# Kernel tuning notes

Measured on AMD Instinct MI355X. Metric: run time of the kernel, lower is better.

## Reference

```python
import jax, jax.numpy as jnp
import numpy as np

EMBED = 1024
HEADS = 16
HEAD_DIM = EMBED // HEADS
N, L = 2, 2048


def setup_inputs() -> dict:
    key = jax.random.key(0)
    ks = jax.random.split(key, 9)
    s = 0.02
    return {
        "values": jax.random.normal(ks[0], (N, L, EMBED), jnp.float32),
        "key": jax.random.normal(ks[1], (N, L, EMBED), jnp.float32),
        "query": jax.random.normal(ks[2], (N, L, EMBED), jnp.float32),
        "mask": jnp.ones((N, 1, 1, L), jnp.int32),
        "Wv": jax.random.normal(ks[3], (HEAD_DIM, HEAD_DIM), jnp.float32) * s,
        "Wk": jax.random.normal(ks[4], (HEAD_DIM, HEAD_DIM), jnp.float32) * s,
        "Wq": jax.random.normal(ks[5], (HEAD_DIM, HEAD_DIM), jnp.float32) * s,
        "bq": jax.random.normal(ks[6], (HEAD_DIM,), jnp.float32) * s,
        "Wo": jax.random.normal(ks[7], (EMBED, EMBED), jnp.float32) * s,
        "bo": jax.random.normal(ks[8], (EMBED,), jnp.float32) * s,
    }


def reference(values, key, query, mask, Wv, Wk, Wq, bq, Wo, bo):
    n, q_len, E = query.shape
    D = Wv.shape[0]
    H = E // D
    # split heads: (N, len, H, D)
    v = values.reshape(n, -1, H, D)
    k = key.reshape(n, -1, H, D)
    q = query.reshape(n, q_len, H, D)
    # per-head linear projections (torch Linear: x @ W.T [+ b])
    v = jnp.einsum("nlhd,ed->nlhe", v, Wv)
    k = jnp.einsum("nlhd,ed->nlhe", k, Wk)
    q = jnp.einsum("nlhd,ed->nlhe", q, Wq) + bq
    # scores: (N, H, q_len, k_len)
    energy = jnp.einsum("nqhd,nkhd->nhqk", q, k)
    energy = jnp.where(mask == 0, jnp.float32(-1e20), energy)
    # NOTE: original scales by sqrt(embed_size), not sqrt(head_dim)
    attn = jax.nn.softmax(energy / jnp.sqrt(jnp.float32(E)), axis=-1)
    out = jnp.einsum("nhqk,nkhd->nqhd", attn, v).reshape(n, q_len, E)
    return out @ Wo.T + bo
```

## Files before the change

kernel.cpp:

```cpp
#include <hip/hip_runtime.h>
#include <hip/hip_bf16.h>
#include <string.h>

#define NB   2
#define SEQ  2048
#define EMB  1024
#define NH   16
#define HD   64
#define SCALE 0.03125f
#define MADD  -3.125e18f

typedef __attribute__((ext_vector_type(8))) short short8;
typedef __attribute__((ext_vector_type(4))) float f32x4;

#define MFMA(a, b, c) __builtin_amdgcn_mfma_f32_16x16x32_bf16(a, b, c, 0, 0, 0)

__device__ __forceinline__ unsigned short f2bf(float x) {
    union { float f; unsigned u; } v; v.f = x;
    unsigned r = v.u + 0x7fffu + ((v.u >> 16) & 1u);
    return (unsigned short)(r >> 16);
}
__device__ __forceinline__ unsigned packbf2(float a, float b) {
    __hip_bfloat162 h = __float22bfloat162_rn(make_float2(a, b));
    unsigned u; memcpy(&u, &h, 4);
    return u;
}

__global__ __launch_bounds__(256) void cvt_wo_kernel(
    const float* __restrict__ Wo, unsigned short* __restrict__ Wob)
{
    int idx = blockIdx.x * 256 + threadIdx.x;
    float4 w = ((const float4*)Wo)[idx];
    uint2 p; p.x = packbf2(w.x, w.y); p.y = packbf2(w.z, w.w);
    ((uint2*)Wob)[idx] = p;
}

__global__ __launch_bounds__(256) void qkv_kernel(
    const float* __restrict__ Qin, const float* __restrict__ Kin,
    const float* __restrict__ Vin,
    const float* __restrict__ Wq, const float* __restrict__ Wk,
    const float* __restrict__ Wv, const float* __restrict__ bq,
    unsigned short* __restrict__ Qp, unsigned short* __restrict__ Kp,
    unsigned short* __restrict__ Vtp)
{
    const int lt = blockIdx.x;
    const int h  = blockIdx.y;
    const int tz = blockIdx.z;
    const int t  = tz >> 1;
    const int n  = tz & 1;

    const float* X; const float* W;
    if (t == 0)      { X = Qin; W = Wq; }
    else if (t == 1) { X = Kin; W = Wk; }
    else             { X = Vin; W = Wv; }

    __shared__ __align__(16) unsigned short sX[64][72];
    __shared__ __align__(16) unsigned short sW[64][72];
    __shared__ __align__(16) unsigned short sT[64][72];

    const int tid  = threadIdx.x;
    const int wave = tid >> 6, lane = tid & 63;
    const int ln   = lane & 15, quad = lane >> 4;

    #pragma unroll
    for (int i = 0; i < 4; ++i) {
        int flat = tid + i * 256;
        int r = flat >> 4, c4 = flat & 15;
        float4 xv = *(const float4*)(X + ((size_t)(n * SEQ + lt * 64 + r)) * EMB + h * HD + c4 * 4);
        uint2 xp; xp.x = packbf2(xv.x, xv.y); xp.y = packbf2(xv.z, xv.w);
        *(uint2*)&sX[r][c4 * 4] = xp;
        float4 wv = *(const float4*)(W + r * HD + c4 * 4);
        uint2 wp; wp.x = packbf2(wv.x, wv.y); wp.y = packbf2(wv.z, wv.w);
        *(uint2*)&sW[r][c4 * 4] = wp;
    }
    __syncthreads();

    short8 af0 = *(const short8*)&sX[wave * 16 + ln][quad * 8];
    short8 af1 = *(const short8*)&sX[wave * 16 + ln][32 + quad * 8];

    f32x4 acc[4];
    #pragma unroll
    for (int nt = 0; nt < 4; ++nt) {
        short8 bf0 = *(const short8*)&sW[nt * 16 + ln][quad * 8];
        short8 bf1 = *(const short8*)&sW[nt * 16 + ln][32 + quad * 8];
        f32x4 a = {0.f, 0.f, 0.f, 0.f};
        a = MFMA(af0, bf0, a);
        a = MFMA(af1, bf1, a);
        acc[nt] = a;
    }

    if (t == 0) {
        #pragma unroll
        for (int nt = 0; nt < 4; ++nt) {
            float bb = bq[nt * 16 + ln];
            #pragma unroll
            for (int a = 0; a < 4; ++a) acc[nt][a] = (acc[nt][a] + bb) * SCALE;
        }
    }

    if (t < 2) {
        unsigned short* Out = (t == 0) ? Qp : Kp;
        #pragma unroll
        for (int a = 0; a < 4; ++a) {
            size_t row = (size_t)((n * NH + h) * SEQ + lt * 64 + wave * 16 + quad * 4 + a);
            #pragma unroll
            for (int nt = 0; nt < 4; ++nt)
                Out[row * HD + nt * 16 + ln] = f2bf(acc[nt][a]);
        }
    } else {
        #pragma unroll
        for (int nt = 0; nt < 4; ++nt)
            #pragma unroll
            for (int a = 0; a < 4; ++a)
                sT[nt * 16 + ln][wave * 16 + quad * 4 + a] = f2bf(acc[nt][a]);
        __syncthreads();
        #pragma unroll
        for (int i = 0; i < 2; ++i) {
            int flat = tid + i * 256;
            int r = flat >> 3, c8 = flat & 7;
            *(float4*)(Vtp + ((size_t)((n * NH + h) * HD + r)) * SEQ + lt * 64 + c8 * 8) =
                *(const float4*)&sT[r][c8 * 8];
        }
    }
}

__global__ __launch_bounds__(128, 2) void flash_kernel(
    const unsigned short* __restrict__ Qp, const unsigned short* __restrict__ Kp,
    const unsigned short* __restrict__ Vtp, const int* __restrict__ mask,
    unsigned short* __restrict__ A )
{
    const int nh = blockIdx.x;
    const int qt = blockIdx.y;
    const int n  = nh >> 4, h = nh & 15;

    const int tid  = threadIdx.x;
    const int wave = tid >> 6, lane = tid & 63;
    const int ln   = lane & 15, quad = lane >> 4;

    __shared__ __align__(16) unsigned short sK [64][72];
    __shared__ __align__(16) unsigned short sVt[64][72];
    __shared__ __align__(16) unsigned short sP [64][72];
    __shared__ float sMadd[SEQ];

    for (int i = tid; i < SEQ; i += 128)
        sMadd[i] = mask[n * SEQ + i] ? 0.f : MADD;

    const unsigned short* Qb = Qp + ((size_t)nh * SEQ + qt * 64 + wave * 32) * HD;
    short8 qf0[2], qf1[2];
    #pragma unroll
    for (int set = 0; set < 2; ++set) {
        qf0[set] = *(const short8*)(Qb + (set * 16 + ln) * HD + quad * 8);
        qf1[set] = *(const short8*)(Qb + (set * 16 + ln) * HD + 32 + quad * 8);
    }

    const unsigned short* Kb = Kp  + (size_t)nh * SEQ * HD;
    const unsigned short* Vb = Vtp + (size_t)nh * HD * SEQ;

    f32x4 o[2][4];
    #pragma unroll
    for (int s2 = 0; s2 < 2; ++s2)
        #pragma unroll
        for (int dt = 0; dt < 4; ++dt) o[s2][dt] = (f32x4){0.f, 0.f, 0.f, 0.f};
    float lsum[2] = {0.f, 0.f};

    for (int kt = 0; kt < SEQ / 64; ++kt) {
        __syncthreads();
        #pragma unroll
        for (int i = 0; i < 4; ++i) {
            int flat = tid + i * 128; int r = flat >> 3, c8 = flat & 7;
            *(float4*)&sK [r][c8 * 8] = *(const float4*)(Kb + ((size_t)(kt * 64 + r)) * HD + c8 * 8);
            *(float4*)&sVt[r][c8 * 8] = *(const float4*)(Vb + (size_t)r * SEQ + kt * 64 + c8 * 8);
        }
        __syncthreads();

        f32x4 s[2][4];
        #pragma unroll
        for (int nt = 0; nt < 4; ++nt) {
            short8 kf0 = *(const short8*)&sK[nt * 16 + ln][quad * 8];
            short8 kf1 = *(const short8*)&sK[nt * 16 + ln][32 + quad * 8];
            f32x4 z0 = {0.f, 0.f, 0.f, 0.f};
            f32x4 z1 = {0.f, 0.f, 0.f, 0.f};
            z0 = MFMA(kf0, qf0[0], z0);
            z0 = MFMA(kf1, qf1[0], z0);
            z1 = MFMA(kf0, qf0[1], z1);
            z1 = MFMA(kf1, qf1[1], z1);
            s[0][nt] = z0; s[1][nt] = z1;
        }

        #pragma unroll
        for (int set = 0; set < 2; ++set) {
            #pragma unroll
            for (int nt = 0; nt < 4; ++nt) {
                float4 md = *(const float4*)&sMadd[kt * 64 + nt * 16 + quad * 4];
                float p0 = __expf(fminf(s[set][nt][0] + md.x, 60.f));
                float p1 = __expf(fminf(s[set][nt][1] + md.y, 60.f));
                float p2 = __expf(fminf(s[set][nt][2] + md.z, 60.f));
                float p3 = __expf(fminf(s[set][nt][3] + md.w, 60.f));
                lsum[set] += (p0 + p1) + (p2 + p3);
                uint2 w; w.x = packbf2(p0, p1); w.y = packbf2(p2, p3);
                *(uint2*)&sP[wave * 32 + set * 16 + ln][nt * 16 + quad * 4] = w;
            }
        }
        asm volatile("s_waitcnt lgkmcnt(0)" ::: "memory");

        short8 vf0[4], vf1[4];
        #pragma unroll
        for (int dt = 0; dt < 4; ++dt) {
            vf0[dt] = *(const short8*)&sVt[dt * 16 + ln][quad * 8];
            vf1[dt] = *(const short8*)&sVt[dt * 16 + ln][32 + quad * 8];
        }
        #pragma unroll
        for (int set = 0; set < 2; ++set) {
            short8 pf0 = *(const short8*)&sP[wave * 32 + set * 16 + ln][quad * 8];
            short8 pf1 = *(const short8*)&sP[wave * 32 + set * 16 + ln][32 + quad * 8];
            #pragma unroll
            for (int dt = 0; dt < 4; ++dt) {
                o[set][dt] = MFMA(pf0, vf0[dt], o[set][dt]);
                o[set][dt] = MFMA(pf1, vf1[dt], o[set][dt]);
            }
        }
    }

    #pragma unroll
    for (int set = 0; set < 2; ++set) {
        float l = lsum[set];
        l += __shfl_xor(l, 16);
        l += __shfl_xor(l, 32);
        #pragma unroll
        for (int a = 0; a < 4; ++a) {
            float lr  = __shfl(l, (lane & 48) | (quad * 4 + a));
            float inv = 1.0f / lr;
            size_t row = (size_t)(n * SEQ + qt * 64 + wave * 32 + set * 16 + quad * 4 + a);
            #pragma unroll
            for (int dt = 0; dt < 4; ++dt)
                A[row * EMB + h * HD + dt * 16 + ln] = f2bf(o[set][dt][a] * inv);
        }
    }
}

__global__ __launch_bounds__(256) void outproj_kernel(
    const unsigned short* __restrict__ A, const unsigned short* __restrict__ Wob,
    const float* __restrict__ bo, float* __restrict__ Out)
{
    const int ct = blockIdx.x;
    const int rt = blockIdx.y;

    const int tid  = threadIdx.x;
    const int wave = tid >> 6, lane = tid & 63;
    const int ln   = lane & 15, quad = lane >> 4;

    __shared__ __align__(16) unsigned short sA[64][72];
    __shared__ __align__(16) unsigned short sW[64][72];

    f32x4 acc[4];
    #pragma unroll
    for (int nt = 0; nt < 4; ++nt) acc[nt] = (f32x4){0.f, 0.f, 0.f, 0.f};

    for (int kc = 0; kc < EMB / 64; ++kc) {
        __syncthreads();
        #pragma unroll
        for (int i = 0; i < 2; ++i) {
            int flat = tid + i * 256; int r = flat >> 3, c8 = flat & 7;
            *(float4*)&sA[r][c8 * 8] =
                *(const float4*)(A + (size_t)(rt * 64 + r) * EMB + kc * 64 + c8 * 8);
            *(float4*)&sW[r][c8 * 8] =
                *(const float4*)(Wob + (size_t)(ct * 64 + r) * EMB + kc * 64 + c8 * 8);
        }
        __syncthreads();

        short8 af0 = *(const short8*)&sA[wave * 16 + ln][quad * 8];
        short8 af1 = *(const short8*)&sA[wave * 16 + ln][32 + quad * 8];
        #pragma unroll
        for (int nt = 0; nt < 4; ++nt) {
            short8 bf0 = *(const short8*)&sW[nt * 16 + ln][quad * 8];
            short8 bf1 = *(const short8*)&sW[nt * 16 + ln][32 + quad * 8];
            acc[nt] = MFMA(af0, bf0, acc[nt]);
            acc[nt] = MFMA(af1, bf1, acc[nt]);
        }
    }

    #pragma unroll
    for (int nt = 0; nt < 4; ++nt) {
        float bb = bo[ct * 64 + nt * 16 + ln];
        #pragma unroll
        for (int a = 0; a < 4; ++a) {
            size_t row = (size_t)(rt * 64 + wave * 16 + quad * 4 + a);
            Out[row * EMB + ct * 64 + nt * 16 + ln] = acc[nt][a] + bb;
        }
    }
}

extern "C" void kernel_launch(void* const* d_in, const int* in_sizes, int n_in,
                              void* d_out, int out_size, void* d_ws, size_t ws_size,
                              hipStream_t stream) {
    const float* values = (const float*)d_in[0];
    const float* key_   = (const float*)d_in[1];
    const float* query  = (const float*)d_in[2];
    const int*   mask   = (const int*)d_in[3];
    const float* Wv     = (const float*)d_in[4];
    const float* Wk     = (const float*)d_in[5];
    const float* Wq     = (const float*)d_in[6];
    const float* bq     = (const float*)d_in[7];
    const float* Wo     = (const float*)d_in[8];
    const float* bo     = (const float*)d_in[9];
    float* out = (float*)d_out;

    unsigned short* ws = (unsigned short*)d_ws;
    const size_t NHLD = (size_t)NB * NH * SEQ * HD;
    unsigned short* Qp    = ws;
    unsigned short* Kp    = ws + NHLD;
    unsigned short* Vtp   = ws + 2 * NHLD;
    unsigned short* Aattn = ws + 3 * NHLD;
    unsigned short* Wob   = ws + 4 * NHLD;

    cvt_wo_kernel<<<dim3(1024), 256, 0, stream>>>(Wo, Wob);
    qkv_kernel<<<dim3(SEQ / 64, NH, 3 * NB), 256, 0, stream>>>(
        query, key_, values, Wq, Wk, Wv, bq, Qp, Kp, Vtp);
    flash_kernel<<<dim3(NB * NH, SEQ / 64), 128, 0, stream>>>(
        Qp, Kp, Vtp, mask, Aattn);
    outproj_kernel<<<dim3(EMB / 64, NB * SEQ / 64), 256, 0, stream>>>(
        Aattn, Wob, bo, out);
}
```

Before: 217.2 us.

## Split flash attention over key range with atomic combine and precompute bf16 weights

Splits the key loop of the flash kernel into two halves across a new grid dimension, accumulating unnormalized outputs and row sums with float atomics into a zeroed workspace, then normalizes and converts to bf16 in a new combine kernel. The projection weights and mask-additive vector are precomputed once in a merged conversion kernel. The QKV kernel now processes 128 rows per block with weights held in registers, and shared-memory row padding changes from 72 to 70. The split raises the number of blocks, at the cost of a memset, atomic traffic on fp32 partials, and an extra kernel launch.

```diff
diff --git a/kernel.cpp b/kernel.cpp
--- a/kernel.cpp
+++ b/kernel.cpp
@@ -9,6 +9,7 @@
 #define HD   64
 #define SCALE 0.03125f
 #define MADD  -3.125e18f
+#define KSPLIT 2
 
 typedef __attribute__((ext_vector_type(8))) short short8;
 typedef __attribute__((ext_vector_type(4))) float f32x4;
@@ -26,124 +27,152 @@
     return u;
 }
 
-__global__ __launch_bounds__(256) void cvt_wo_kernel(
-    const float* __restrict__ Wo, unsigned short* __restrict__ Wob)
-{
-    int idx = blockIdx.x * 256 + threadIdx.x;
-    float4 w = ((const float4*)Wo)[idx];
-    uint2 p; p.x = packbf2(w.x, w.y); p.y = packbf2(w.z, w.w);
-    ((uint2*)Wob)[idx] = p;
+__global__ __launch_bounds__(256) void cvt_kernel(
+    const float* __restrict__ Wo, const float* __restrict__ Wq,
+    const float* __restrict__ Wk, const float* __restrict__ Wv,
+    const int* __restrict__ mask,
+    unsigned short* __restrict__ Wob, unsigned short* __restrict__ Wqb,
+    unsigned short* __restrict__ Wkb, unsigned short* __restrict__ Wvb,
+    float* __restrict__ maddG)
+{
+    const int b = blockIdx.x, tid = threadIdx.x;
+    if (b < 1024) {
+        int idx = b * 256 + tid;
+        float4 w = ((const float4*)Wo)[idx];
+        uint2 p; p.x = packbf2(w.x, w.y); p.y = packbf2(w.z, w.w);
+        ((uint2*)Wob)[idx] = p;
+    } else if (b < 1027) {
+        const float* W = (b == 1024) ? Wq : (b == 1025) ? Wk : Wv;
+        unsigned short* Wb = (b == 1024) ? Wqb : (b == 1025) ? Wkb : Wvb;
+        #pragma unroll
+        for (int i = 0; i < 4; ++i) {
+            int idx = tid + i * 256;
+            float4 w = ((const float4*)W)[idx];
+            uint2 p; p.x = packbf2(w.x, w.y); p.y = packbf2(w.z, w.w);
+            ((uint2*)Wb)[idx] = p;
+        }
+    } else {
+        #pragma unroll
+        for (int i = 0; i < 16; ++i) {
+            int idx = tid + i * 256;
+            maddG[idx] = mask[idx] ? 0.f : MADD;
+        }
+    }
 }
 
 __global__ __launch_bounds__(256) void qkv_kernel(
     const float* __restrict__ Qin, const float* __restrict__ Kin,
     const float* __restrict__ Vin,
-    const float* __restrict__ Wq, const float* __restrict__ Wk,
-    const float* __restrict__ Wv, const float* __restrict__ bq,
+    const unsigned short* __restrict__ Wqb, const unsigned short* __restrict__ Wkb,
+    const unsigned short* __restrict__ Wvb, const float* __restrict__ bq,
     unsigned short* __restrict__ Qp, unsigned short* __restrict__ Kp,
     unsigned short* __restrict__ Vtp)
 {
     const int lt = blockIdx.x;
     const int h  = blockIdx.y;
     const int tz = blockIdx.z;
-    const int t  = tz >> 1;
-    const int n  = tz & 1;
-
-    const float* X; const float* W;
-    if (t == 0)      { X = Qin; W = Wq; }
-    else if (t == 1) { X = Kin; W = Wk; }
-    else             { X = Vin; W = Wv; }
-
-    __shared__ __align__(16) unsigned short sX[64][72];
-    __shared__ __align__(16) unsigned short sW[64][72];
-    __shared__ __align__(16) unsigned short sT[64][72];
+    const int t  = tz >> 1, n = tz & 1;
+
+    const float* X; const unsigned short* Wb;
+    if (t == 0)      { X = Qin; Wb = Wqb; }
+    else if (t == 1) { X = Kin; Wb = Wkb; }
+    else             { X = Vin; Wb = Wvb; }
+
+    __shared__ __align__(16) unsigned short sX[128][70];
+    __shared__ __align__(16) unsigned short sT[64][136];
+
+    const int tid = threadIdx.x, wave = tid >> 6, lane = tid & 63;
+    const int ln = lane & 15, quad = lane >> 4;
+
+    #pragma unroll
+    for (int i = 0; i < 8; ++i) {
+        int flat = tid + i * 256;
+        int r = flat >> 4, c4 = flat & 15;
+        float4 xv = *(const float4*)(X + ((size_t)(n * SEQ + lt * 128 + r)) * EMB + h * HD + c4 * 4);
+        uint2 xp; xp.x = packbf2(xv.x, xv.y); xp.y = packbf2(xv.z, xv.w);
+        *(uint2*)&sX[r][c4 * 4] = xp;
+    }
+    short8 wf0[4], wf1[4];
+    #pragma unroll
+    for (int nt = 0; nt < 4; ++nt) {
+        wf0[nt] = *(const short8*)(Wb + (nt * 16 + ln) * HD + quad * 8);
+        wf1[nt] = *(const short8*)(Wb + (nt * 16 + ln) * HD + 32 + quad * 8);
+    }
+    __syncthreads();
+
+    f32x4 acc[2][4];
+    #pragma unroll
+    for (int set = 0; set < 2; ++set) {
+        short8 af0 = *(const short8*)&sX[wave * 32 + set * 16 + ln][quad * 8];
+        short8 af1 = *(const short8*)&sX[wave * 32 + set * 16 + ln][32 + quad * 8];
+        #pragma unroll
+        for (int nt = 0; nt < 4; ++nt) {
+            f32x4 a = {0.f, 0.f, 0.f, 0.f};
+            a = MFMA(af0, wf0[nt], a);
+            a = MFMA(af1, wf1[nt], a);
+            acc[set][nt] = a;
+        }
+    }
+
+    if (t == 0) {
+        #pragma unroll
+        for (int nt = 0; nt < 4; ++nt) {
+            float bb = bq[nt * 16 + ln];
+            #pragma unroll
+            for (int set = 0; set < 2; ++set)
+                #pragma unroll
+                for (int a = 0; a < 4; ++a)
+                    acc[set][nt][a] = (acc[set][nt][a] + bb) * SCALE;
+        }
+    }
+
+    if (t < 2) {
+        unsigned short* Out = (t == 0) ? Qp : Kp;
+        #pragma unroll
+        for (int set = 0; set < 2; ++set)
+            #pragma unroll
+            for (int a = 0; a < 4; ++a) {
+                size_t row = (size_t)((n * NH + h) * SEQ + lt * 128 + wave * 32 + set * 16 + quad * 4 + a);
+                #pragma unroll
+                for (int nt = 0; nt < 4; ++nt)
+                    Out[row * HD + nt * 16 + ln] = f2bf(acc[set][nt][a]);
+            }
+    } else {
+        #pragma unroll
+        for (int set = 0; set < 2; ++set)
+            #pragma unroll
+            for (int nt = 0; nt < 4; ++nt)
+                #pragma unroll
+                for (int a = 0; a < 4; ++a)
+                    sT[nt * 16 + ln][wave * 32 + set * 16 + quad * 4 + a] = f2bf(acc[set][nt][a]);
+        __syncthreads();
+        #pragma unroll
+        for (int i = 0; i < 4; ++i) {
+            int flat = tid + i * 256;
+            int r = flat >> 4, c8 = flat & 15;
+            *(float4*)(Vtp + ((size_t)((n * NH + h) * HD + r)) * SEQ + lt * 128 + c8 * 8) =
+                *(const float4*)&sT[r][c8 * 8];
+        }
+    }
+}
+
+__global__ __launch_bounds__(128, 3) void flash_kernel(
+    const unsigned short* __restrict__ Qp, const unsigned short* __restrict__ Kp,
+    const unsigned short* __restrict__ Vtp, const float* __restrict__ maddG,
+    float* __restrict__ Opart, float* __restrict__ lpart)
+{
+    const int nh = blockIdx.x;
+    const int qt = blockIdx.y;
+    const int z  = blockIdx.z;
+    const int n  = nh >> 4;
 
     const int tid  = threadIdx.x;
     const int wave = tid >> 6, lane = tid & 63;
     const int ln   = lane & 15, quad = lane >> 4;
 
-    #pragma unroll
-    for (int i = 0; i < 4; ++i) {
-        int flat = tid + i * 256;
-        int r = flat >> 4, c4 = flat & 15;
-        float4 xv = *(const float4*)(X + ((size_t)(n * SEQ + lt * 64 + r)) * EMB + h * HD + c4 * 4);
-        uint2 xp; xp.x = packbf2(xv.x, xv.y); xp.y = packbf2(xv.z, xv.w);
-        *(uint2*)&sX[r][c4 * 4] = xp;
-        float4 wv = *(const float4*)(W + r * HD + c4 * 4);
-        uint2 wp; wp.x = packbf2(wv.x, wv.y); wp.y = packbf2(wv.z, wv.w);
-        *(uint2*)&sW[r][c4 * 4] = wp;
-    }
-    __syncthreads();
-
-    short8 af0 = *(const short8*)&sX[wave * 16 + ln][quad * 8];
-    short8 af1 = *(const short8*)&sX[wave * 16 + ln][32 + quad * 8];
-
-    f32x4 acc[4];
-    #pragma unroll
-    for (int nt = 0; nt < 4; ++nt) {
-        short8 bf0 = *(const short8*)&sW[nt * 16 + ln][quad * 8];
-        short8 bf1 = *(const short8*)&sW[nt * 16 + ln][32 + quad * 8];
-        f32x4 a = {0.f, 0.f, 0.f, 0.f};
-        a = MFMA(af0, bf0, a);
-        a = MFMA(af1, bf1, a);
-        acc[nt] = a;
-    }
-
-    if (t == 0) {
-        #pragma unroll
-        for (int nt = 0; nt < 4; ++nt) {
-            float bb = bq[nt * 16 + ln];
-            #pragma unroll
-            for (int a = 0; a < 4; ++a) acc[nt][a] = (acc[nt][a] + bb) * SCALE;
-        }
-    }
-
-    if (t < 2) {
-        unsigned short* Out = (t == 0) ? Qp : Kp;
-        #pragma unroll
-        for (int a = 0; a < 4; ++a) {
-            size_t row = (size_t)((n * NH + h) * SEQ + lt * 64 + wave * 16 + quad * 4 + a);
-            #pragma unroll
-            for (int nt = 0; nt < 4; ++nt)
-                Out[row * HD + nt * 16 + ln] = f2bf(acc[nt][a]);
-        }
-    } else {
-        #pragma unroll
-        for (int nt = 0; nt < 4; ++nt)
-            #pragma unroll
-            for (int a = 0; a < 4; ++a)
-                sT[nt * 16 + ln][wave * 16 + quad * 4 + a] = f2bf(acc[nt][a]);
-        __syncthreads();
-        #pragma unroll
-        for (int i = 0; i < 2; ++i) {
-            int flat = tid + i * 256;
-            int r = flat >> 3, c8 = flat & 7;
-            *(float4*)(Vtp + ((size_t)((n * NH + h) * HD + r)) * SEQ + lt * 64 + c8 * 8) =
-                *(const float4*)&sT[r][c8 * 8];
-        }
-    }
-}
-
-__global__ __launch_bounds__(128, 2) void flash_kernel(
-    const unsigned short* __restrict__ Qp, const unsigned short* __restrict__ Kp,
-    const unsigned short* __restrict__ Vtp, const int* __restrict__ mask,
-    unsigned short* __restrict__ A )
-{
-    const int nh = blockIdx.x;
-    const int qt = blockIdx.y;
-    const int n  = nh >> 4, h = nh & 15;
-
-    const int tid  = threadIdx.x;
-    const int wave = tid >> 6, lane = tid & 63;
-    const int ln   = lane & 15, quad = lane >> 4;
-
-    __shared__ __align__(16) unsigned short sK [64][72];
-    __shared__ __align__(16) unsigned short sVt[64][72];
-    __shared__ __align__(16) unsigned short sP [64][72];
-    __shared__ float sMadd[SEQ];
-
-    for (int i = tid; i < SEQ; i += 128)
-        sMadd[i] = mask[n * SEQ + i] ? 0.f : MADD;
+    __shared__ __align__(16) unsigned short sK [64][70];
+    __shared__ __align__(16) unsigned short sVt[64][70];
+    __shared__ __align__(16) unsigned short sP [64][70];
 
     const unsigned short* Qb = Qp + ((size_t)nh * SEQ + qt * 64 + wave * 32) * HD;
     short8 qf0[2], qf1[2];
@@ -155,6 +184,7 @@
 
     const unsigned short* Kb = Kp  + (size_t)nh * SEQ * HD;
     const unsigned short* Vb = Vtp + (size_t)nh * HD * SEQ;
+    const float* mb = maddG + n * SEQ;
 
     f32x4 o[2][4];
     #pragma unroll
@@ -163,7 +193,7 @@
         for (int dt = 0; dt < 4; ++dt) o[s2][dt] = (f32x4){0.f, 0.f, 0.f, 0.f};
     float lsum[2] = {0.f, 0.f};
 
-    for (int kt = 0; kt < SEQ / 64; ++kt) {
+    for (int kt = z * (SEQ / 64 / KSPLIT); kt < (z + 1) * (SEQ / 64 / KSPLIT); ++kt) {
         __syncthreads();
         #pragma unroll
         for (int i = 0; i < 4; ++i) {
@@ -171,6 +201,10 @@
             *(float4*)&sK [r][c8 * 8] = *(const float4*)(Kb + ((size_t)(kt * 64 + r)) * HD + c8 * 8);
             *(float4*)&sVt[r][c8 * 8] = *(const float4*)(Vb + (size_t)r * SEQ + kt * 64 + c8 * 8);
         }
+        float4 mdv[4];
+        #pragma unroll
+        for (int nt = 0; nt < 4; ++nt)
+            mdv[nt] = *(const float4*)(mb + kt * 64 + nt * 16 + quad * 4);
         __syncthreads();
 
         f32x4 s[2][4];
@@ -191,11 +225,10 @@
         for (int set = 0; set < 2; ++set) {
             #pragma unroll
             for (int nt = 0; nt < 4; ++nt) {
-                float4 md = *(const float4*)&sMadd[kt * 64 + nt * 16 + quad * 4];
-                float p0 = __expf(fminf(s[set][nt][0] + md.x, 60.f));
-                float p1 = __expf(fminf(s[set][nt][1] + md.y, 60.f));
-                float p2 = __expf(fminf(s[set][nt][2] + md.z, 60.f));
-                float p3 = __expf(fminf(s[set][nt][3] + md.w, 60.f));
+                float p0 = __expf(fminf(s[set][nt][0] + mdv[nt].x, 60.f));
+                float p1 = __expf(fminf(s[set][nt][1] + mdv[nt].y, 60.f));
+                float p2 = __expf(fminf(s[set][nt][2] + mdv[nt].z, 60.f));
+                float p3 = __expf(fminf(s[set][nt][3] + mdv[nt].w, 60.f));
                 lsum[set] += (p0 + p1) + (p2 + p3);
                 uint2 w; w.x = packbf2(p0, p1); w.y = packbf2(p2, p3);
                 *(uint2*)&sP[wave * 32 + set * 16 + ln][nt * 16 + quad * 4] = w;
@@ -221,21 +254,35 @@
         }
     }
 
+    const size_t rb = (size_t)nh * SEQ + qt * 64 + wave * 32;
     #pragma unroll
     for (int set = 0; set < 2; ++set) {
         float l = lsum[set];
         l += __shfl_xor(l, 16);
         l += __shfl_xor(l, 32);
+        if (quad == 0) atomicAdd(&lpart[rb + set * 16 + ln], l);
         #pragma unroll
         for (int a = 0; a < 4; ++a) {
-            float lr  = __shfl(l, (lane & 48) | (quad * 4 + a));
-            float inv = 1.0f / lr;
-            size_t row = (size_t)(n * SEQ + qt * 64 + wave * 32 + set * 16 + quad * 4 + a);
+            size_t row = rb + set * 16 + quad * 4 + a;
             #pragma unroll
             for (int dt = 0; dt < 4; ++dt)
-                A[row * EMB + h * HD + dt * 16 + ln] = f2bf(o[set][dt][a] * inv);
-        }
-    }
+                atomicAdd(&Opart[row * HD + dt * 16 + ln], o[set][dt][a]);
+        }
+    }
+}
+
+__global__ __launch_bounds__(256) void combine_kernel(
+    const float* __restrict__ Opart, const float* __restrict__ lpart,
+    unsigned short* __restrict__ Aattn)
+{
+    int idx = blockIdx.x * 256 + threadIdx.x;
+    int row = idx >> 4, d4 = idx & 15;
+    float4 ov = ((const float4*)Opart)[idx];
+    float inv = 1.0f / lpart[row];
+    int n = row >> 15, h = (row >> 11) & 15, l = row & 2047;
+    uint2 p; p.x = packbf2(ov.x * inv, ov.y * inv);
+    p.y = packbf2(ov.z * inv, ov.w * inv);
+    *(uint2*)(Aattn + ((size_t)(n * SEQ + l)) * EMB + h * HD + d4 * 4) = p;
 }
 
 __global__ __launch_bounds__(256) void outproj_kernel(
@@ -249,8 +296,8 @@
     const int wave = tid >> 6, lane = tid & 63;
     const int ln   = lane & 15, quad = lane >> 4;
 
-    __shared__ __align__(16) unsigned short sA[64][72];
-    __shared__ __align__(16) unsigned short sW[64][72];
+    __shared__ __align__(16) unsigned short sA[64][70];
+    __shared__ __align__(16) unsigned short sW[64][70];
 
     f32x4 acc[4];
     #pragma unroll
@@ -305,19 +352,31 @@
     const float* bo     = (const float*)d_in[9];
     float* out = (float*)d_out;
 
-    unsigned short* ws = (unsigned short*)d_ws;
     const size_t NHLD = (size_t)NB * NH * SEQ * HD;
-    unsigned short* Qp    = ws;
-    unsigned short* Kp    = ws + NHLD;
-    unsigned short* Vtp   = ws + 2 * NHLD;
-    unsigned short* Aattn = ws + 3 * NHLD;
-    unsigned short* Wob   = ws + 4 * NHLD;
-
-    cvt_wo_kernel<<<dim3(1024), 256, 0, stream>>>(Wo, Wob);
-    qkv_kernel<<<dim3(SEQ / 64, NH, 3 * NB), 256, 0, stream>>>(
-        query, key_, values, Wq, Wk, Wv, bq, Qp, Kp, Vtp);
-    flash_kernel<<<dim3(NB * NH, SEQ / 64), 128, 0, stream>>>(
-        Qp, Kp, Vtp, mask, Aattn);
+
+    float* wsf   = (float*)d_ws;
+    float* Opart = wsf;
+    float* lpart = wsf + NHLD;
+    unsigned short* ws2 = (unsigned short*)(wsf + NHLD + NB * NH * SEQ);
+    unsigned short* Qp    = ws2;
+    unsigned short* Kp    = ws2 + NHLD;
+    unsigned short* Vtp   = ws2 + 2 * NHLD;
+    unsigned short* Aattn = ws2 + 3 * NHLD;
+    unsigned short* Wob   = ws2 + 4 * NHLD;
+    unsigned short* Wqb   = Wob + (size_t)EMB * EMB;
+    unsigned short* Wkb   = Wqb + HD * HD;
+    unsigned short* Wvb   = Wkb + HD * HD;
+    float* maddG = (float*)(Wvb + HD * HD);
+
+    hipMemsetAsync(d_ws, 0, (NHLD + (size_t)NB * NH * SEQ) * sizeof(float), stream);
+
+    cvt_kernel<<<dim3(1028), 256, 0, stream>>>(
+        Wo, Wq, Wk, Wv, mask, Wob, Wqb, Wkb, Wvb, maddG);
+    qkv_kernel<<<dim3(SEQ / 128, NH, 3 * NB), 256, 0, stream>>>(
+        query, key_, values, Wqb, Wkb, Wvb, bq, Qp, Kp, Vtp);
+    flash_kernel<<<dim3(NB * NH, SEQ / 64, KSPLIT), 128, 0, stream>>>(
+        Qp, Kp, Vtp, maddG, Opart, lpart);
+    combine_kernel<<<dim3(4096), 256, 0, stream>>>(Opart, lpart, Aattn);
     outproj_kernel<<<dim3(EMB / 64, NB * SEQ / 64), 256, 0, stream>>>(
         Aattn, Wob, bo, out);
 }
```

Result: slower. 246.1 us (+13.3%).
